# Kernel tuning notes

Measured on AMD Instinct MI355X. Metric: run time of the kernel, lower is better.

Reference implementation:

```python
import jax, jax.numpy as jnp
import numpy as np

BEAM = 4
START = 1


def setup_inputs() -> dict:
    key = jax.random.key(0)
    ks = jax.random.split(key, 10)
    S, B, H, E, V = 32, 16, 1024, 256, 32000
    Din = E + E + H  # embed + enc_input_step + enc_output_step
    sc = 0.02
    return {
        "enc_h_n": jax.random.normal(ks[0], (1, B, H), jnp.float32),
        "enc_c_n": jax.random.normal(ks[1], (1, B, H), jnp.float32),
        "enc_outputs": jax.random.normal(ks[2], (S, B, H), jnp.float32),
        "enc_inputs": jax.random.normal(ks[3], (S, B, E), jnp.float32),
        "embed": jax.random.normal(ks[4], (V, E), jnp.float32) * sc,
        "w_ih": jax.random.normal(ks[5], (Din, 4 * H), jnp.float32) * sc,
        "w_hh": jax.random.normal(ks[6], (H, 4 * H), jnp.float32) * sc,
        "b_lstm": jnp.zeros((4 * H,), jnp.float32),
        "w_out": jax.random.normal(ks[7], (H, V), jnp.float32) * sc,
        "b_out": jnp.zeros((V,), jnp.float32),
    }


def reference(enc_h_n, enc_c_n, enc_outputs, enc_inputs,
              embed, w_ih, w_hh, b_lstm, w_out, b_out):
    S, B, _ = enc_inputs.shape
    H = enc_h_n.shape[2]
    V = w_out.shape[1]
    K = BEAM

    def decode(word, h, c, ein, eout):
        # word: [B] int, h/c: [B,H], ein: [B,E], eout: [B,H]
        x = jnp.concatenate([embed[word], ein, eout], axis=-1)  # [B,Din]
        gates = x @ w_ih + h @ w_hh + b_lstm                    # [B,4H]
        i, f, g, o = jnp.split(gates, 4, axis=-1)
        c2 = jax.nn.sigmoid(f) * c + jax.nn.sigmoid(i) * jnp.tanh(g)
        h2 = jax.nn.sigmoid(o) * jnp.tanh(c2)
        logits = h2 @ w_out + b_out                             # [B,V]
        return logits, h2, c2

    # ---- init_beam_search (step 0) ----
    h0, c0 = enc_h_n[0], enc_c_n[0]
    word0 = jnp.full((B,), START, dtype=jnp.int32)
    logits0, h1, c1 = decode(word0, h0, c0, enc_inputs[0], enc_outputs[0])
    probs0 = jax.nn.softmax(logits0, axis=-1)
    top_v, top_i = jax.lax.top_k(probs0, K)  # [B,K]
    # NOTE: original code never updates current_scores inside the loop -> constant
    scores = top_v

    h = jnp.broadcast_to(h1, (K, B, H)) + 0.0  # per-beam hidden state copies
    c = jnp.broadcast_to(c1, (K, B, H)) + 0.0
    word = top_i  # [B,K]

    decode_beams = jax.vmap(decode, in_axes=(1, 0, 0, None, None))

    def step(carry, xs):
        h, c, word = carry
        ein, eout = xs
        logits, h2, c2 = decode_beams(word, h, c, ein, eout)  # [K,B,V]
        probs = jax.nn.softmax(logits, axis=-1)
        # space_search layout: beam b occupies cols [b*V, (b+1)*V); tile repeats
        # each beam score V times -> equivalent to broadcast over vocab axis.
        space = jnp.transpose(probs, (1, 0, 2)) * scores[:, :, None]  # [B,K,V]
        _, ti = jax.lax.top_k(space.reshape(B, K * V), K)             # [B,K]
        word2 = ti % V
        return (h2, c2, word2), ti

    (_, _, _), tis = jax.lax.scan(step, (h, c, word),
                                  (enc_inputs[1:], enc_outputs[1:]))
    out = jnp.concatenate([top_i[None], tis], axis=0)  # [S,B,K]
    return jnp.transpose(out, (2, 1, 0)).astype(jnp.int32)  # [K,B,S]
```

## Files before the change

kernel.cpp:

```cpp
#include <hip/hip_runtime.h>
#include <math.h>

#define S_LEN 32
#define B_N   16
#define H_N   1024
#define E_N   256
#define V_N   32000
#define KBEAM 4
#define DIN   1536
#define D2    2560
#define R_N   64
#define NDS   20
#define NB    500

typedef _Float16 f16;
typedef f16   f16x8 __attribute__((ext_vector_type(8)));
typedef float f32x4 __attribute__((ext_vector_type(4)));
#define MFMA(A,B,C) __builtin_amdgcn_mfma_f32_16x16x32_f16(A,B,C,0,0,0)

__device__ __forceinline__ float sigmf(float x){ return 1.0f/(1.0f+expf(-x)); }
__device__ __forceinline__ bool better(float v1,int i1,float v2,int i2){
  return (v1>v2) || (v1==v2 && i1<i2);
}
__device__ __forceinline__ void ins4(float bv,int bi,
    float&av0,float&av1,float&av2,float&av3,int&ai0,int&ai1,int&ai2,int&ai3){
  if (better(bv,bi,av3,ai3)){ av3=bv; ai3=bi;
    if (better(av3,ai3,av2,ai2)){ float t=av2;av2=av3;av3=t; int q=ai2;ai2=ai3;ai3=q;
      if (better(av2,ai2,av1,ai1)){ t=av1;av1=av2;av2=t; q=ai1;ai1=ai2;ai2=q;
        if (better(av1,ai1,av0,ai0)){ t=av0;av0=av1;av1=t; q=ai0;ai0=ai1;ai1=q; } } } }
}

__device__ __forceinline__ void packx(f16* xpk, int r, int k, float v){
  int m = r >> 4, lm = r & 15;
  int ks = k >> 5, kq = (k & 31) >> 3, i = k & 7;
  int l = lm + 16*kq;
  size_t base = (((size_t)m*80 + ks)*2)*512 + l*8 + i;
  f16 hh = (f16)v;
  xpk[base]       = hh;
  xpk[base + 512] = (f16)((v - (float)hh)*4096.0f);
}

#define FMA16(w4, h4) { \
  acc[0][0]=fmaf(w4.x,h4.x,acc[0][0]); acc[0][1]=fmaf(w4.x,h4.y,acc[0][1]); \
  acc[0][2]=fmaf(w4.x,h4.z,acc[0][2]); acc[0][3]=fmaf(w4.x,h4.w,acc[0][3]); \
  acc[1][0]=fmaf(w4.y,h4.x,acc[1][0]); acc[1][1]=fmaf(w4.y,h4.y,acc[1][1]); \
  acc[1][2]=fmaf(w4.y,h4.z,acc[1][2]); acc[1][3]=fmaf(w4.y,h4.w,acc[1][3]); \
  acc[2][0]=fmaf(w4.z,h4.x,acc[2][0]); acc[2][1]=fmaf(w4.z,h4.y,acc[2][1]); \
  acc[2][2]=fmaf(w4.z,h4.z,acc[2][2]); acc[2][3]=fmaf(w4.z,h4.w,acc[2][3]); \
  acc[3][0]=fmaf(w4.w,h4.x,acc[3][0]); acc[3][1]=fmaf(w4.w,h4.y,acc[3][1]); \
  acc[3][2]=fmaf(w4.w,h4.z,acc[3][2]); acc[3][3]=fmaf(w4.w,h4.w,acc[3][3]); }

#define LOADSET(S, s) { size_t o_ = (size_t)(s)*1024; \
  Bh##S  = *(const f16x8*)(wp + o_);  Bl##S  = *(const f16x8*)(wp + o_ + 512); \
  A0h##S = *(const f16x8*)(hp0 + o_); A0l##S = *(const f16x8*)(hp0 + o_ + 512); \
  A1h##S = *(const f16x8*)(hp1 + o_); A1l##S = *(const f16x8*)(hp1 + o_ + 512); \
  A2h##S = *(const f16x8*)(hp2 + o_); A2l##S = *(const f16x8*)(hp2 + o_ + 512); \
  A3h##S = *(const f16x8*)(hp3 + o_); A3l##S = *(const f16x8*)(hp3 + o_ + 512); }
#define COMPSET(S) { \
  c10 = MFMA(A0h##S, Bh##S, c10); c20 = MFMA(A0l##S, Bh##S, c20); c20 = MFMA(A0h##S, Bl##S, c20); \
  c11 = MFMA(A1h##S, Bh##S, c11); c21 = MFMA(A1l##S, Bh##S, c21); c21 = MFMA(A1h##S, Bl##S, c21); \
  c12 = MFMA(A2h##S, Bh##S, c12); c22 = MFMA(A2l##S, Bh##S, c22); c22 = MFMA(A2h##S, Bl##S, c22); \
  c13 = MFMA(A3h##S, Bh##S, c13); c23 = MFMA(A3l##S, Bh##S, c23); c23 = MFMA(A3h##S, Bl##S, c23); }
#define DECLFRAGS \
  f32x4 c10={0,0,0,0}, c11={0,0,0,0}, c12={0,0,0,0}, c13={0,0,0,0}; \
  f32x4 c20={0,0,0,0}, c21={0,0,0,0}, c22={0,0,0,0}, c23={0,0,0,0}; \
  f16x8 Bh0,Bl0,A0h0,A1h0,A2h0,A3h0,A0l0,A1l0,A2l0,A3l0; \
  f16x8 Bh1,Bl1,A0h1,A1h1,A2h1,A3h1,A0l1,A1l1,A2l1,A3l1;

__global__ __launch_bounds__(256) void k_init(
    const float* __restrict__ enc_h_n, const float* __restrict__ enc_c_n,
    const float* __restrict__ enc_outputs, const float* __restrict__ enc_inputs,
    const float* __restrict__ embed, float* __restrict__ x, float* __restrict__ c,
    f16* __restrict__ xpk){
  int r = blockIdx.x, tid = threadIdx.x, b = r & 15;
  float* xr = x + (size_t)r*D2;
  float v0 = embed[E_N + tid];
  float v1 = enc_inputs[b*E_N + tid];
  xr[tid]       = v0;
  xr[E_N + tid] = v1;
  float eo[4], hh[4];
  #pragma unroll
  for (int q=0;q<4;++q){
    eo[q] = enc_outputs[b*H_N + q*256 + tid];
    hh[q] = enc_h_n[b*H_N + q*256 + tid];
    xr[2*E_N + q*256 + tid] = eo[q];
    xr[DIN + q*256 + tid]   = hh[q];
    c[(size_t)r*H_N + q*256 + tid] = enc_c_n[b*H_N + q*256 + tid];
  }
  if (xpk){
    packx(xpk, r, tid, v0);
    packx(xpk, r, E_N + tid, v1);
    #pragma unroll
    for (int q=0;q<4;++q){
      packx(xpk, r, 2*E_N + q*256 + tid, eo[q]);
      packx(xpk, r, DIN + q*256 + tid,   hh[q]);
    }
  }
}

__global__ __launch_bounds__(256) void k_convw(
    const float* __restrict__ w, f16* __restrict__ wpk){
  __shared__ f16 Th[64][66];
  __shared__ f16 Tl[64][66];
  int v0 = blockIdx.x*64, d0 = blockIdx.y*64;
  int tid = threadIdx.x;
  int r = tid >> 4, cq = (tid & 15)*4;
  #pragma unroll
  for (int rr=0; rr<4; ++rr){
    int d = r + rr*16;
    float4 x = *(const float4*)&w[(size_t)(d0+d)*V_N + v0 + cq];
    f16 h;
    h=(f16)x.x; Th[d][cq+0]=h; Tl[d][cq+0]=(f16)((x.x-(float)h)*4096.0f);
    h=(f16)x.y; Th[d][cq+1]=h; Tl[d][cq+1]=(f16)((x.y-(float)h)*4096.0f);
    h=(f16)x.z; Th[d][cq+2]=h; Tl[d][cq+2]=(f16)((x.z-(float)h)*4096.0f);
    h=(f16)x.w; Th[d][cq+3]=h; Tl[d][cq+3]=(f16)((x.w-(float)h)*4096.0f);
  }
  __syncthreads();
  int T2 = tid >> 6, l = tid & 63;
  int lm = l & 15, kq = l >> 4;
  int Tg = blockIdx.x*4 + T2;
  #pragma unroll
  for (int ks2=0; ks2<2; ++ks2){
    int ksg = blockIdx.y*2 + ks2;
    f16x8 a, b2;
    #pragma unroll
    for (int i=0;i<8;++i){
      int dd = ks2*32 + kq*8 + i;
      a[i]  = Th[dd][T2*16 + lm];
      b2[i] = Tl[dd][T2*16 + lm];
    }
    size_t base = ((size_t)(Tg*32 + ksg)*2)*512 + l*8;
    *(f16x8*)&wpk[base]       = a;
    *(f16x8*)&wpk[base + 512] = b2;
  }
}

__global__ __launch_bounds__(256) void k_convg(
    const float* __restrict__ w_ih, const float* __restrict__ w_hh,
    f16* __restrict__ wgpk){
  __shared__ f16 Th[64][66];
  __shared__ f16 Tl[64][66];
  int jb = blockIdx.x*16, k0 = blockIdx.y*64;
  int tid = threadIdx.x;
  int r = tid >> 4;
  int g = (tid & 15) >> 2, q = tid & 3;
  #pragma unroll
  for (int rr=0; rr<4; ++rr){
    int d = r + rr*16;
    int row = k0 + d;
    const float* src = (row < DIN) ? &w_ih[(size_t)row*4096 + g*1024 + jb + q*4]
                                   : &w_hh[(size_t)(row-DIN)*4096 + g*1024 + jb + q*4];
    float4 x = *(const float4*)src;
    f16 h;
    h=(f16)x.x; Th[d][(q*4+0)*4+g]=h; Tl[d][(q*4+0)*4+g]=(f16)((x.x-(float)h)*4096.0f);
    h=(f16)x.y; Th[d][(q*4+1)*4+g]=h; Tl[d][(q*4+1)*4+g]=(f16)((x.y-(float)h)*4096.0f);
    h=(f16)x.z; Th[d][(q*4+2)*4+g]=h; Tl[d][(q*4+2)*4+g]=(f16)((x.z-(float)h)*4096.0f);
    h=(f16)x.w; Th[d][(q*4+3)*4+g]=h; Tl[d][(q*4+3)*4+g]=(f16)((x.w-(float)h)*4096.0f);
  }
  __syncthreads();
  int T2 = tid >> 6, l = tid & 63;
  int lm = l & 15, kq = l >> 4;
  int Tg = blockIdx.x*4 + T2;
  #pragma unroll
  for (int ks2=0; ks2<2; ++ks2){
    int ksg = blockIdx.y*2 + ks2;
    f16x8 a, b2;
    #pragma unroll
    for (int i=0;i<8;++i){
      int dd = ks2*32 + kq*8 + i;
      a[i]  = Th[dd][T2*16 + lm];
      b2[i] = Tl[dd][T2*16 + lm];
    }
    size_t base = (((size_t)Tg*80 + ksg)*2)*512 + l*8;
    *(f16x8*)&wgpk[base]       = a;
    *(f16x8*)&wgpk[base + 512] = b2;
  }
}

__global__ __launch_bounds__(256) void k_cell(
    const f16* __restrict__ wgpk, const f16* __restrict__ xpk_cur,
    const float* __restrict__ b_lstm, float* __restrict__ c,
    f16* __restrict__ xpk_next){
  int tid = threadIdx.x;
  int lane = tid & 63;
  int wv = tid >> 6;
  int T  = blockIdx.x;
  int ksb = wv*20;

  const f16* wp  = wgpk    + (((size_t)T*80 + ksb)*2)*512 + lane*8;
  const f16* hp0 = xpk_cur + (((size_t)0*80 + ksb)*2)*512 + lane*8;
  const f16* hp1 = xpk_cur + (((size_t)1*80 + ksb)*2)*512 + lane*8;
  const f16* hp2 = xpk_cur + (((size_t)2*80 + ksb)*2)*512 + lane*8;
  const f16* hp3 = xpk_cur + (((size_t)3*80 + ksb)*2)*512 + lane*8;

  DECLFRAGS

  LOADSET(0, 0)
  for (int s=0; s<20; s+=2){
    LOADSET(1, s+1)
    COMPSET(0)
    if (s+2<20) LOADSET(0, s+2)
    COMPSET(1)
  }

  __shared__ float Gs[4][64][17];
  const float inv = 1.0f/4096.0f;
  int lm = lane & 15;
  int rb2 = (lane>>4)*4;
#define CSTT(mt, A1, A2) { \
  _Pragma("unroll") for (int rg=0; rg<4; ++rg){ \
    Gs[wv][(mt)*16 + rb2 + rg][lm] = A1[rg] + A2[rg]*inv; } }
  CSTT(0, c10, c20) CSTT(1, c11, c21) CSTT(2, c12, c22) CSTT(3, c13, c23)
  __syncthreads();

  int r = tid >> 2, u = tid & 3;
  int j = T*4 + u;
  float gi = Gs[0][r][u*4+0] + Gs[1][r][u*4+0] + Gs[2][r][u*4+0] + Gs[3][r][u*4+0] + b_lstm[j];
  float gf = Gs[0][r][u*4+1] + Gs[1][r][u*4+1] + Gs[2][r][u*4+1] + Gs[3][r][u*4+1] + b_lstm[1024+j];
  float gg = Gs[0][r][u*4+2] + Gs[1][r][u*4+2] + Gs[2][r][u*4+2] + Gs[3][r][u*4+2] + b_lstm[2048+j];
  float go = Gs[0][r][u*4+3] + Gs[1][r][u*4+3] + Gs[2][r][u*4+3] + Gs[3][r][u*4+3] + b_lstm[3072+j];
  float cv = c[(size_t)r*H_N + j];
  float c2v = sigmf(gf)*cv + sigmf(gi)*tanhf(gg);
  float h2 = sigmf(go)*tanhf(c2v);
  c[(size_t)r*H_N + j] = c2v;
  packx(xpk_next, r, DIN + j, h2);
}

#define GWLD(d, off) (*(const float4*)((((d) < DIN) ? (w_ih + (size_t)(d)*4096) \
                       : (w_hh + (size_t)((d)-DIN)*4096)) + (off)))
__global__ __launch_bounds__(256) void k_gates(
    const float* __restrict__ x, const float* __restrict__ w_ih,
    const float* __restrict__ w_hh, float* __restrict__ gpart){
  int tid = threadIdx.x;
  int jt = blockIdx.x, ks = blockIdx.y;
  int cx = tid & 15, ry = tid >> 4;
  int cb = jt*64;
  int wdd = tid >> 4, wseg = tid & 15;
  int xrow = tid >> 3, xseg = tid & 7;

  __shared__ float Wt0[32][64], Wt1[32][64];
  __shared__ float Xt0[32][68], Xt1[32][68];

  float acc[4][4];
  #pragma unroll
  for (int cc=0;cc<4;++cc)
    #pragma unroll
    for (int rr=0;rr<4;++rr) acc[cc][rr]=0.f;

  int d0 = ks*128;
  const float* xp0 = x + (size_t)xrow*D2 + d0 + xseg*4;
  const float* xp1 = x + (size_t)(xrow+32)*D2 + d0 + xseg*4;

#define GLQ(WA,WB,X0,X1, ch) { int d_ = d0 + (ch)*32; \
  WA = GWLD(d_+wdd,    cb+wseg*4); \
  WB = GWLD(d_+16+wdd, cb+wseg*4); \
  X0 = *(const float4*)(xp0 + (ch)*32); \
  X1 = *(const float4*)(xp1 + (ch)*32); }
#define GSQ(Wt,Xt, WA,WB,X0,X1) { \
  *(float4*)&Wt[wdd][wseg*4]    = WA; \
  *(float4*)&Wt[wdd+16][wseg*4] = WB; \
  Xt[xseg*4+0][xrow] = X0.x; Xt[xseg*4+1][xrow] = X0.y; \
  Xt[xseg*4+2][xrow] = X0.z; Xt[xseg*4+3][xrow] = X0.w; \
  Xt[xseg*4+0][xrow+32] = X1.x; Xt[xseg*4+1][xrow+32] = X1.y; \
  Xt[xseg*4+2][xrow+32] = X1.z; Xt[xseg*4+3][xrow+32] = X1.w; }
#define GCQ(Wt,Xt) { _Pragma("unroll 8") for (int dd=0; dd<32; ++dd){ \
    float4 w4 = *(const float4*)&Wt[dd][cx*4]; \
    float4 h4 = *(const float4*)&Xt[dd][ry*4]; \
    FMA16(w4, h4) } }

  float4 wA0,wB0,x00,x10, wA1,wB1,x01,x11;
  GLQ(wA0,wB0,x00,x10, 0)
  GSQ(Wt0,Xt0, wA0,wB0,x00,x10)
  GLQ(wA1,wB1,x01,x11, 1)
  __syncthreads();

  for (int ch=0; ch<4; ch+=2){
    if (ch+2<4) GLQ(wA0,wB0,x00,x10, ch+2)
    GSQ(Wt1,Xt1, wA1,wB1,x01,x11)
    GCQ(Wt0,Xt0)
    __syncthreads();
    if (ch+3<4) GLQ(wA1,wB1,x01,x11, ch+3)
    if (ch+2<4) GSQ(Wt0,Xt0, wA0,wB0,x00,x10)
    GCQ(Wt1,Xt1)
    if (ch+2<4) __syncthreads();
  }
  #pragma unroll
  for (int rr=0;rr<4;++rr){
    float4 o; o.x=acc[0][rr]; o.y=acc[1][rr]; o.z=acc[2][rr]; o.w=acc[3][rr];
    *(float4*)&gpart[((size_t)(ks*R_N + ry*4+rr))*4096 + cb + cx*4] = o;
  }
}

__global__ __launch_bounds__(256) void k_lstm(
    const float* __restrict__ gpart, const float* __restrict__ b_lstm,
    float* __restrict__ c, float* __restrict__ xn, float* __restrict__ h2t,
    int nds){
  int r = blockIdx.x, tid = threadIdx.x;
  int j = blockIdx.y*256 + tid;
  float gi = b_lstm[j], gf = b_lstm[1024+j], gg = b_lstm[2048+j], go = b_lstm[3072+j];
  for (int ds=0; ds<nds; ++ds){
    size_t base = ((size_t)ds*R_N + r)*4096;
    gi += gpart[base + j];      gf += gpart[base + 1024 + j];
    gg += gpart[base + 2048+j]; go += gpart[base + 3072 + j];
  }
  float cv = c[(size_t)r*H_N + j];
  float c2 = sigmf(gf)*cv + sigmf(gi)*tanhf(gg);
  float h2 = sigmf(go)*tanhf(c2);
  c[(size_t)r*H_N + j] = c2;
  xn[(size_t)r*D2 + DIN + j] = h2;
  h2t[(size_t)j*R_N + r] = h2;
}

__global__ __launch_bounds__(256) void k_logits_mfma(
    const f16* __restrict__ wpk, const f16* __restrict__ xpk_next,
    const float* __restrict__ b_out,
    float* __restrict__ pm, float* __restrict__ pz,
    float* __restrict__ pv, int* __restrict__ pi){
  int tid = threadIdx.x;
  int lane = tid & 63;
  int wv = tid >> 6;
  int T  = blockIdx.x*4 + wv;
  int vb = T*16;

  const f16* wp  = wpk + ((size_t)(T*32))*2*512 + lane*8;
  const f16* hp0 = xpk_next + (((size_t)0*80 + 48)*2)*512 + lane*8;
  const f16* hp1 = xpk_next + (((size_t)1*80 + 48)*2)*512 + lane*8;
  const f16* hp2 = xpk_next + (((size_t)2*80 + 48)*2)*512 + lane*8;
  const f16* hp3 = xpk_next + (((size_t)3*80 + 48)*2)*512 + lane*8;

  DECLFRAGS

  LOADSET(0, 0)
  for (int s=0; s<32; s+=2){
    LOADSET(1, s+1)
    COMPSET(0)
    if (s+2<32) LOADSET(0, s+2)
    COMPSET(1)
  }

  __shared__ float Ls[64][68];

  const float inv = 1.0f/4096.0f;
  int lm = lane & 15;
  int rb = (lane>>4)*4;
  float bias = b_out[vb + lm];
#define STT(mt, A1, A2) { \
  _Pragma("unroll") for (int rg=0; rg<4; ++rg){ \
    Ls[(mt)*16 + rb + rg][wv*16 + lm] = A1[rg] + A2[rg]*inv + bias; } }
  STT(0, c10, c20) STT(1, c11, c21) STT(2, c12, c22) STT(3, c13, c23)
  __syncthreads();

  int cx = tid & 15, ry = tid >> 4;
  int cb = blockIdx.x * 64;
  #pragma unroll
  for (int rr=0;rr<4;++rr){
    int row = ry*4 + rr;
    float v0 = Ls[row][cx*4+0], v1 = Ls[row][cx*4+1];
    float v2 = Ls[row][cx*4+2], v3 = Ls[row][cx*4+3];
    int   c0i = cb + cx*4;
    float tv0=-INFINITY,tv1=-INFINITY,tv2=-INFINITY,tv3=-INFINITY;
    int   ti0=0x7fffffff,ti1=0x7fffffff,ti2=0x7fffffff,ti3=0x7fffffff;
    ins4(v0,c0i+0,tv0,tv1,tv2,tv3,ti0,ti1,ti2,ti3);
    ins4(v1,c0i+1,tv0,tv1,tv2,tv3,ti0,ti1,ti2,ti3);
    ins4(v2,c0i+2,tv0,tv1,tv2,tv3,ti0,ti1,ti2,ti3);
    ins4(v3,c0i+3,tv0,tv1,tv2,tv3,ti0,ti1,ti2,ti3);
    float z = expf(v0-tv0)+expf(v1-tv0)+expf(v2-tv0)+expf(v3-tv0);
    #pragma unroll
    for (int msk=1; msk<16; msk<<=1){
      float om  = __shfl_xor(tv0, msk, 16);
      float oz  = __shfl_xor(z,   msk, 16);
      float ov1 = __shfl_xor(tv1, msk, 16);
      float ov2 = __shfl_xor(tv2, msk, 16);
      float ov3 = __shfl_xor(tv3, msk, 16);
      int   oi0 = __shfl_xor(ti0, msk, 16);
      int   oi1 = __shfl_xor(ti1, msk, 16);
      int   oi2 = __shfl_xor(ti2, msk, 16);
      int   oi3 = __shfl_xor(ti3, msk, 16);
      float M = fmaxf(tv0, om);
      z = z*expf(tv0-M) + oz*expf(om-M);
      ins4(om, oi0, tv0,tv1,tv2,tv3, ti0,ti1,ti2,ti3);
      ins4(ov1,oi1, tv0,tv1,tv2,tv3, ti0,ti1,ti2,ti3);
      ins4(ov2,oi2, tv0,tv1,tv2,tv3, ti0,ti1,ti2,ti3);
      ins4(ov3,oi3, tv0,tv1,tv2,tv3, ti0,ti1,ti2,ti3);
    }
    if (cx == 0){
      size_t base = (size_t)row*NB + blockIdx.x;
      pm[base]=tv0; pz[base]=z;
      pv[base*4+0]=tv0; pv[base*4+1]=tv1; pv[base*4+2]=tv2; pv[base*4+3]=tv3;
      pi[base*4+0]=ti0; pi[base*4+1]=ti1; pi[base*4+2]=ti2; pi[base*4+3]=ti3;
    }
  }
}

__global__ __launch_bounds__(256) void k_logits_fused(
    const float* __restrict__ h2t, const float* __restrict__ w_out,
    const float* __restrict__ b_out,
    float* __restrict__ pm, float* __restrict__ pz,
    float* __restrict__ pv, int* __restrict__ pi){
  int tid = threadIdx.x;
  int cx  = tid & 15, ry = tid >> 4;
  int cb  = blockIdx.x * 64;
  int sdd = tid >> 4, seg = tid & 15;
  __shared__ float Wt[32][64];
  __shared__ float Ht[32][64];
  float acc[4][4];
  #pragma unroll
  for (int cc=0;cc<4;++cc)
    #pragma unroll
    for (int rr=0;rr<4;++rr) acc[cc][rr]=0.f;
  const float* gW = w_out + (size_t)sdd*V_N + cb + seg*4;
  const float* gH = h2t + sdd*64 + seg*4;
#define FLQ(WA,WB,HA,HB, ch) { \
  const float* gWn = gW + (size_t)(ch)*32*V_N; \
  const float* gHn = gH + (size_t)(ch)*32*64; \
  WA = *(const float4*)gWn; WB = *(const float4*)(gWn + (size_t)16*V_N); \
  HA = *(const float4*)gHn; HB = *(const float4*)(gHn + 16*64); }
#define FSQ(WA,WB,HA,HB) { \
  *(float4*)&Wt[sdd][seg*4]    = WA; \
  *(float4*)&Wt[sdd+16][seg*4] = WB; \
  *(float4*)&Ht[sdd][seg*4]    = HA; \
  *(float4*)&Ht[sdd+16][seg*4] = HB; }
#define FCQ() { _Pragma("unroll 8") for (int dd=0; dd<32; ++dd){ \
    float4 w4 = *(const float4*)&Wt[dd][cx*4]; \
    float4 h4 = *(const float4*)&Ht[dd][ry*4]; \
    FMA16(w4, h4) } }
  float4 wA0,wB0,hA0,hB0, wA1,wB1,hA1,hB1;
  FLQ(wA0,wB0,hA0,hB0, 0)
  FSQ(wA0,wB0,hA0,hB0)
  FLQ(wA1,wB1,hA1,hB1, 1)
  __syncthreads();
  for (int ch=0; ch<32; ch+=2){
    if (ch+2<32) FLQ(wA0,wB0,hA0,hB0, ch+2)
    FCQ()
    __syncthreads();
    FSQ(wA1,wB1,hA1,hB1)
    __syncthreads();
    if (ch+3<32) FLQ(wA1,wB1,hA1,hB1, ch+3)
    FCQ()
    if (ch+2<32){
      __syncthreads();
      FSQ(wA0,wB0,hA0,hB0)
      __syncthreads();
    }
  }
  float4 bias = *(const float4*)&b_out[cb + cx*4];
  #pragma unroll
  for (int rr=0;rr<4;++rr){
    float v0 = acc[0][rr]+bias.x, v1 = acc[1][rr]+bias.y;
    float v2 = acc[2][rr]+bias.z, v3 = acc[3][rr]+bias.w;
    int   c0i = cb + cx*4;
    float tv0=-INFINITY,tv1=-INFINITY,tv2=-INFINITY,tv3=-INFINITY;
    int   ti0=0x7fffffff,ti1=0x7fffffff,ti2=0x7fffffff,ti3=0x7fffffff;
    ins4(v0,c0i+0,tv0,tv1,tv2,tv3,ti0,ti1,ti2,ti3);
    ins4(v1,c0i+1,tv0,tv1,tv2,tv3,ti0,ti1,ti2,ti3);
    ins4(v2,c0i+2,tv0,tv1,tv2,tv3,ti0,ti1,ti2,ti3);
    ins4(v3,c0i+3,tv0,tv1,tv2,tv3,ti0,ti1,ti2,ti3);
    float z = expf(v0-tv0)+expf(v1-tv0)+expf(v2-tv0)+expf(v3-tv0);
    #pragma unroll
    for (int msk=1; msk<16; msk<<=1){
      float om  = __shfl_xor(tv0, msk, 16);
      float oz  = __shfl_xor(z,   msk, 16);
      float ov1 = __shfl_xor(tv1, msk, 16);
      float ov2 = __shfl_xor(tv2, msk, 16);
      float ov3 = __shfl_xor(tv3, msk, 16);
      int   oi0 = __shfl_xor(ti0, msk, 16);
      int   oi1 = __shfl_xor(ti1, msk, 16);
      int   oi2 = __shfl_xor(ti2, msk, 16);
      int   oi3 = __shfl_xor(ti3, msk, 16);
      float M = fmaxf(tv0, om);
      z = z*expf(tv0-M) + oz*expf(om-M);
      ins4(om, oi0, tv0,tv1,tv2,tv3, ti0,ti1,ti2,ti3);
      ins4(ov1,oi1, tv0,tv1,tv2,tv3, ti0,ti1,ti2,ti3);
      ins4(ov2,oi2, tv0,tv1,tv2,tv3, ti0,ti1,ti2,ti3);
      ins4(ov3,oi3, tv0,tv1,tv2,tv3, ti0,ti1,ti2,ti3);
    }
    if (cx == 0){
      int row = ry*4 + rr;
      size_t base = (size_t)row*NB + blockIdx.x;
      pm[base]=tv0; pz[base]=z;
      pv[base*4+0]=tv0; pv[base*4+1]=tv1; pv[base*4+2]=tv2; pv[base*4+3]=tv3;
      pi[base*4+0]=ti0; pi[base*4+1]=ti1; pi[base*4+2]=ti2; pi[base*4+3]=ti3;
    }
  }
}

__global__ __launch_bounds__(256) void k_final(
    const float* __restrict__ pm, const float* __restrict__ pz,
    const float* __restrict__ pv, const int* __restrict__ pi,
    float* __restrict__ scores, int* __restrict__ out, int t,
    float* __restrict__ xn, f16* __restrict__ xpk_next,
    const float* __restrict__ enc_inputs, const float* __restrict__ enc_outputs,
    const float* __restrict__ embed){
  int b = blockIdx.x, tid = threadIdx.x;
  int kk = tid >> 6, lane = tid & 63;
  __shared__ float fM[KBEAM], fZ[KBEAM], fV[16];
  __shared__ int   fI[16], sw[KBEAM];
  int nk = (t==0) ? 1 : KBEAM;
  if (kk < nk){
    size_t rb = (size_t)(kk*B_N + b)*NB;
    float m=-INFINITY, z=0.f;
    float av0=-INFINITY,av1=-INFINITY,av2=-INFINITY,av3=-INFINITY;
    int   ai0=0x7fffffff,ai1=0x7fffffff,ai2=0x7fffffff,ai3=0x7fffffff;
    for (int p0=lane; p0<NB; p0+=64){
      size_t p = rb + p0;
      float mf = pm[p];
      float M = fmaxf(m, mf);
      z = z*expf(m-M) + pz[p]*expf(mf-M);
      m = M;
      #pragma unroll
      for (int q=0;q<4;++q)
        ins4(pv[p*4+q], pi[p*4+q], av0,av1,av2,av3, ai0,ai1,ai2,ai3);
    }
    #pragma unroll
    for (int msk=1; msk<64; msk<<=1){
      float om  = __shfl_xor(m,   msk);
      float oz  = __shfl_xor(z,   msk);
      float ov0 = __shfl_xor(av0, msk);
      float ov1 = __shfl_xor(av1, msk);
      float ov2 = __shfl_xor(av2, msk);
      float ov3 = __shfl_xor(av3, msk);
      int   oi0 = __shfl_xor(ai0, msk);
      int   oi1 = __shfl_xor(ai1, msk);
      int   oi2 = __shfl_xor(ai2, msk);
      int   oi3 = __shfl_xor(ai3, msk);
      float M = fmaxf(m, om);
      z = z*expf(m-M) + oz*expf(om-M);
      m = M;
      ins4(ov0,oi0, av0,av1,av2,av3, ai0,ai1,ai2,ai3);
      ins4(ov1,oi1, av0,av1,av2,av3, ai0,ai1,ai2,ai3);
      ins4(ov2,oi2, av0,av1,av2,av3, ai0,ai1,ai2,ai3);
      ins4(ov3,oi3, av0,av1,av2,av3, ai0,ai1,ai2,ai3);
    }
    if (lane == 0){
      fM[kk]=m; fZ[kk]=z;
      fV[kk*4+0]=av0; fV[kk*4+1]=av1; fV[kk*4+2]=av2; fV[kk*4+3]=av3;
      fI[kk*4+0]=ai0; fI[kk*4+1]=ai1; fI[kk*4+2]=ai2; fI[kk*4+3]=ai3;
    }
  }
  __syncthreads();
  if (tid==0){
    if (t==0){
      #pragma unroll
      for (int j=0;j<4;++j){
        float p = expf(fV[j]-fM[0])/fZ[0];
        scores[b*4+j] = p;
        out[j*(B_N*S_LEN) + b*S_LEN] = fI[j];
        sw[j] = fI[j];
      }
    } else {
      float cv[16]; int cj[16];
      for (int k=0;k<4;++k){
        float s = scores[b*4+k];
        #pragma unroll
        for (int j=0;j<4;++j){
          cv[k*4+j] = expf(fV[k*4+j]-fM[k])/fZ[k]*s;
          cj[k*4+j] = k*V_N + fI[k*4+j];
        }
      }
      bool used[16];
      for (int i=0;i<16;++i) used[i]=false;
      for (int rank=0;rank<4;++rank){
        int best=-1;
        for (int i=0;i<16;++i){
          if (used[i]) continue;
          if (best<0 || cv[i]>cv[best] || (cv[i]==cv[best] && cj[i]<cj[best])) best=i;
        }
        used[best]=true;
        out[rank*(B_N*S_LEN) + b*S_LEN + t] = cj[best];
        sw[rank] = cj[best] % V_N;
      }
    }
  }
  __syncthreads();
  if (t < S_LEN-1){
    const float* ein = enc_inputs  + (size_t)(t+1)*B_N*E_N + (size_t)b*E_N;
    const float* eo  = enc_outputs + (size_t)(t+1)*B_N*H_N + (size_t)b*H_N;
    #pragma unroll
    for (int j=0;j<KBEAM;++j){
      int r = j*B_N + b;
      const float* em = embed + (size_t)sw[j]*E_N;
      float v0 = em[tid], v1 = ein[tid];
      if (xpk_next){
        packx(xpk_next, r, tid, v0); packx(xpk_next, r, E_N + tid, v1);
        #pragma unroll
        for (int q=0;q<4;++q) packx(xpk_next, r, 2*E_N + q*256 + tid, eo[q*256 + tid]);
      } else {
        float* xr = xn + (size_t)r*D2;
        xr[tid]       = v0;
        xr[E_N + tid] = v1;
        #pragma unroll
        for (int q=0;q<4;++q) xr[2*E_N + q*256 + tid] = eo[q*256 + tid];
      }
    }
  }
}

extern "C" void kernel_launch(void* const* d_in, const int* in_sizes, int n_in,
                              void* d_out, int out_size, void* d_ws, size_t ws_size,
                              hipStream_t stream) {
  (void)in_sizes; (void)n_in; (void)out_size;
  const float* enc_h_n     = (const float*)d_in[0];
  const float* enc_c_n     = (const float*)d_in[1];
  const float* enc_outputs = (const float*)d_in[2];
  const float* enc_inputs  = (const float*)d_in[3];
  const float* embed       = (const float*)d_in[4];
  const float* w_ih        = (const float*)d_in[5];
  const float* w_hh        = (const float*)d_in[6];
  const float* b_lstm      = (const float*)d_in[7];
  const float* w_out       = (const float*)d_in[8];
  const float* b_out       = (const float*)d_in[9];
  int* out = (int*)d_out;

  float* ws = (float*)d_ws;
  const size_t FRONTF = (size_t)R_N*D2*2 + (size_t)R_N*H_N + (size_t)H_N*R_N;
  const size_t XPKF   = (size_t)R_N*D2;
  const size_t GPARTF = (size_t)NDS*R_N*4096;
  const size_t STATF  = (size_t)R_N*NB*10;
  const size_t WSPLF  = (size_t)V_N*H_N;
  const size_t WGPKF  = (size_t)D2*4096;
  size_t need_split = (FRONTF + 2*XPKF + GPARTF + STATF + 64 + WSPLF + WGPKF)*sizeof(float);
  bool use_split = (ws_size >= need_split);

  float* xA     = ws;
  float* xB     = xA + (size_t)R_N*D2;
  float* cbuf   = xB + (size_t)R_N*D2;
  float* h2t    = cbuf + (size_t)R_N*H_N;
  f16*   xpkA   = (f16*)(h2t + (size_t)H_N*R_N);
  f16*   xpkB   = (f16*)(h2t + (size_t)H_N*R_N + XPKF);
  float* big    = h2t + (size_t)H_N*R_N + 2*XPKF;
  float* gpart  = big;
  float* pm     = big + GPARTF;
  float* pz     = pm + (size_t)R_N*NB;
  float* pv     = pz + (size_t)R_N*NB;
  int*   pi     = (int*)(pv + (size_t)R_N*NB*4);
  float* scoresb= (float*)(pi + (size_t)R_N*NB*4);
  f16*   wpk    = (f16*)(scoresb + 64);
  f16*   wgpk   = (f16*)((float*)(scoresb + 64) + WSPLF);

  if (use_split){
    k_convw<<<dim3(V_N/64, H_N/64), 256, 0, stream>>>(w_out, wpk);
    k_convg<<<dim3(4096/64, D2/64), 256, 0, stream>>>(w_ih, w_hh, wgpk);
  }
  k_init<<<R_N, 256, 0, stream>>>(enc_h_n, enc_c_n, enc_outputs, enc_inputs,
                                  embed, xA, cbuf, use_split ? xpkA : (f16*)0);

  for (int t=0; t<S_LEN; ++t){
    float* xc = (t & 1) ? xB : xA;
    float* xn = (t & 1) ? xA : xB;
    f16* xpk_cur  = (t & 1) ? xpkB : xpkA;
    f16* xpk_next = (t & 1) ? xpkA : xpkB;
    if (use_split){
      k_cell<<<256, 256, 0, stream>>>(wgpk, xpk_cur, b_lstm, cbuf, xpk_next);
      k_logits_mfma<<<NB, 256, 0, stream>>>(wpk, xpk_next, b_out, pm, pz, pv, pi);
      k_final<<<B_N, 256, 0, stream>>>(pm, pz, pv, pi, scoresb, out, t, xn, xpk_next,
                                       enc_inputs, enc_outputs, embed);
    } else {
      k_gates <<<dim3(64, NDS), 256, 0, stream>>>(xc, w_ih, w_hh, gpart);
      k_lstm<<<dim3(R_N, 4), 256, 0, stream>>>(gpart, b_lstm, cbuf, xn, h2t, NDS);
      k_logits_fused<<<NB, 256, 0, stream>>>(h2t, w_out, b_out, pm, pz, pv, pi);
      k_final<<<B_N, 256, 0, stream>>>(pm, pz, pv, pi, scoresb, out, t, xn, (f16*)0,
                                       enc_inputs, enc_outputs, embed);
    }
  }
}
```

Before: 2.733 ms.

## Fuse beam top-k reduction into logits kernel via last-block atomic counter

The logits MFMA kernel now counts finished blocks with an atomic counter per step, and the last 16 blocks to arrive spin until all blocks are done, then do the per-batch softmax/top-k merge and beam selection that k_final used to do. k_final keeps only the gather of next-step inputs, reading the chosen words back from out. This moves the reduction work out of a separate launch, but it spins on a counter that assumes all 500 blocks can be resident at once, and it adds a launch_bounds occupancy hint. It also leaves dead placeholder code at the end of the kernel.

```diff
diff --git a/kernel.cpp b/kernel.cpp
--- a/kernel.cpp
+++ b/kernel.cpp
@@ -311,11 +311,14 @@
   h2t[(size_t)j*R_N + r] = h2;
 }
 
-__global__ __launch_bounds__(256) void k_logits_mfma(
+__global__ __launch_bounds__(256, 2) void k_logits_mfma(
     const f16* __restrict__ wpk, const f16* __restrict__ xpk_next,
     const float* __restrict__ b_out,
     float* __restrict__ pm, float* __restrict__ pz,
-    float* __restrict__ pv, int* __restrict__ pi){
+    float* __restrict__ pv, int* __restrict__ pi,
+    float* __restrict__ scores, int* __restrict__ out, int t,
+    const float* __restrict__ enc_inputs, const float* __restrict__ enc_outputs,
+    const float* __restrict__ embed, unsigned* __restrict__ cnt){
   int tid = threadIdx.x;
   int lane = tid & 63;
   int wv = tid >> 6;
@@ -350,47 +353,154 @@
   STT(0, c10, c20) STT(1, c11, c21) STT(2, c12, c22) STT(3, c13, c23)
   __syncthreads();
 
-  int cx = tid & 15, ry = tid >> 4;
-  int cb = blockIdx.x * 64;
-  #pragma unroll
-  for (int rr=0;rr<4;++rr){
-    int row = ry*4 + rr;
-    float v0 = Ls[row][cx*4+0], v1 = Ls[row][cx*4+1];
-    float v2 = Ls[row][cx*4+2], v3 = Ls[row][cx*4+3];
-    int   c0i = cb + cx*4;
-    float tv0=-INFINITY,tv1=-INFINITY,tv2=-INFINITY,tv3=-INFINITY;
-    int   ti0=0x7fffffff,ti1=0x7fffffff,ti2=0x7fffffff,ti3=0x7fffffff;
-    ins4(v0,c0i+0,tv0,tv1,tv2,tv3,ti0,ti1,ti2,ti3);
-    ins4(v1,c0i+1,tv0,tv1,tv2,tv3,ti0,ti1,ti2,ti3);
-    ins4(v2,c0i+2,tv0,tv1,tv2,tv3,ti0,ti1,ti2,ti3);
-    ins4(v3,c0i+3,tv0,tv1,tv2,tv3,ti0,ti1,ti2,ti3);
-    float z = expf(v0-tv0)+expf(v1-tv0)+expf(v2-tv0)+expf(v3-tv0);
-    #pragma unroll
-    for (int msk=1; msk<16; msk<<=1){
-      float om  = __shfl_xor(tv0, msk, 16);
-      float oz  = __shfl_xor(z,   msk, 16);
-      float ov1 = __shfl_xor(tv1, msk, 16);
-      float ov2 = __shfl_xor(tv2, msk, 16);
-      float ov3 = __shfl_xor(tv3, msk, 16);
-      int   oi0 = __shfl_xor(ti0, msk, 16);
-      int   oi1 = __shfl_xor(ti1, msk, 16);
-      int   oi2 = __shfl_xor(ti2, msk, 16);
-      int   oi3 = __shfl_xor(ti3, msk, 16);
-      float M = fmaxf(tv0, om);
-      z = z*expf(tv0-M) + oz*expf(om-M);
-      ins4(om, oi0, tv0,tv1,tv2,tv3, ti0,ti1,ti2,ti3);
-      ins4(ov1,oi1, tv0,tv1,tv2,tv3, ti0,ti1,ti2,ti3);
-      ins4(ov2,oi2, tv0,tv1,tv2,tv3, ti0,ti1,ti2,ti3);
-      ins4(ov3,oi3, tv0,tv1,tv2,tv3, ti0,ti1,ti2,ti3);
-    }
-    if (cx == 0){
-      size_t base = (size_t)row*NB + blockIdx.x;
-      pm[base]=tv0; pz[base]=z;
-      pv[base*4+0]=tv0; pv[base*4+1]=tv1; pv[base*4+2]=tv2; pv[base*4+3]=tv3;
-      pi[base*4+0]=ti0; pi[base*4+1]=ti1; pi[base*4+2]=ti2; pi[base*4+3]=ti3;
-    }
-  }
-}
+  {
+    int cx = tid & 15, ry = tid >> 4;
+    int cb = blockIdx.x * 64;
+    #pragma unroll
+    for (int rr=0;rr<4;++rr){
+      int row = ry*4 + rr;
+      float v0 = Ls[row][cx*4+0], v1 = Ls[row][cx*4+1];
+      float v2 = Ls[row][cx*4+2], v3 = Ls[row][cx*4+3];
+      int   c0i = cb + cx*4;
+      float tv0=-INFINITY,tv1=-INFINITY,tv2=-INFINITY,tv3=-INFINITY;
+      int   ti0=0x7fffffff,ti1=0x7fffffff,ti2=0x7fffffff,ti3=0x7fffffff;
+      ins4(v0,c0i+0,tv0,tv1,tv2,tv3,ti0,ti1,ti2,ti3);
+      ins4(v1,c0i+1,tv0,tv1,tv2,tv3,ti0,ti1,ti2,ti3);
+      ins4(v2,c0i+2,tv0,tv1,tv2,tv3,ti0,ti1,ti2,ti3);
+      ins4(v3,c0i+3,tv0,tv1,tv2,tv3,ti0,ti1,ti2,ti3);
+      float z = expf(v0-tv0)+expf(v1-tv0)+expf(v2-tv0)+expf(v3-tv0);
+      #pragma unroll
+      for (int msk=1; msk<16; msk<<=1){
+        float om  = __shfl_xor(tv0, msk, 16);
+        float oz  = __shfl_xor(z,   msk, 16);
+        float ov1 = __shfl_xor(tv1, msk, 16);
+        float ov2 = __shfl_xor(tv2, msk, 16);
+        float ov3 = __shfl_xor(tv3, msk, 16);
+        int   oi0 = __shfl_xor(ti0, msk, 16);
+        int   oi1 = __shfl_xor(ti1, msk, 16);
+        int   oi2 = __shfl_xor(ti2, msk, 16);
+        int   oi3 = __shfl_xor(ti3, msk, 16);
+        float M = fmaxf(tv0, om);
+        z = z*expf(tv0-M) + oz*expf(om-M);
+        ins4(om, oi0, tv0,tv1,tv2,tv3, ti0,ti1,ti2,ti3);
+        ins4(ov1,oi1, tv0,tv1,tv2,tv3, ti0,ti1,ti2,ti3);
+        ins4(ov2,oi2, tv0,tv1,tv2,tv3, ti0,ti1,ti2,ti3);
+        ins4(ov3,oi3, tv0,tv1,tv2,tv3, ti0,ti1,ti2,ti3);
+      }
+      if (cx == 0){
+        size_t base = (size_t)row*NB + blockIdx.x;
+        pm[base]=tv0; pz[base]=z;
+        pv[base*4+0]=tv0; pv[base*4+1]=tv1; pv[base*4+2]=tv2; pv[base*4+3]=tv3;
+        pi[base*4+0]=ti0; pi[base*4+1]=ti1; pi[base*4+2]=ti2; pi[base*4+3]=ti3;
+      }
+    }
+  }
+
+  __shared__ unsigned sOld;
+  __syncthreads();
+  if (tid == 0){
+    __threadfence();
+    sOld = atomicAdd(&cnt[t], 1u);
+  }
+  __syncthreads();
+  unsigned old = sOld;
+  if (old < NB-16) return;
+  int b = (int)(old - (NB-16));
+  if (tid == 0){
+    while (atomicAdd(&cnt[t], 0u) < NB) __builtin_amdgcn_s_sleep(8);
+  }
+  __syncthreads();
+  __threadfence();
+
+  int kk = tid >> 6;
+  __shared__ float fM[KBEAM], fZ[KBEAM], fV[16];
+  __shared__ int   fI[16], sw[KBEAM];
+  int nk = (t==0) ? 1 : KBEAM;
+  if (kk < nk){
+    size_t rbb = (size_t)(kk*B_N + b)*NB;
+    float m=-INFINITY, z=0.f;
+    float av0=-INFINITY,av1=-INFINITY,av2=-INFINITY,av3=-INFINITY;
+    int   ai0=0x7fffffff,ai1=0x7fffffff,ai2=0x7fffffff,ai3=0x7fffffff;
+    for (int p0=lane; p0<NB; p0+=64){
+      size_t p = rbb + p0;
+      float mf = pm[p];
+      float M = fmaxf(m, mf);
+      z = z*expf(m-M) + pz[p]*expf(mf-M);
+      m = M;
+      #pragma unroll
+      for (int q=0;q<4;++q)
+        ins4(pv[p*4+q], pi[p*4+q], av0,av1,av2,av3, ai0,ai1,ai2,ai3);
+    }
+    #pragma unroll
+    for (int msk=1; msk<64; msk<<=1){
+      float om  = __shfl_xor(m,   msk);
+      float oz  = __shfl_xor(z,   msk);
+      float ov0 = __shfl_xor(av0, msk);
+      float ov1 = __shfl_xor(av1, msk);
+      float ov2 = __shfl_xor(av2, msk);
+      float ov3 = __shfl_xor(av3, msk);
+      int   oi0 = __shfl_xor(ai0, msk);
+      int   oi1 = __shfl_xor(ai1, msk);
+      int   oi2 = __shfl_xor(ai2, msk);
+      int   oi3 = __shfl_xor(ai3, msk);
+      float M = fmaxf(m, om);
+      z = z*expf(m-M) + oz*expf(om-M);
+      m = M;
+      ins4(ov0,oi0, av0,av1,av2,av3, ai0,ai1,ai2,ai3);
+      ins4(ov1,oi1, av0,av1,av2,av3, ai0,ai1,ai2,ai3);
+      ins4(ov2,oi2, av0,av1,av2,av3, ai0,ai1,ai2,ai3);
+      ins4(ov3,oi3, av0,av1,av2,av3, ai0,ai1,ai2,ai3);
+    }
+    if (lane == 0){
+      fM[kk]=m; fZ[kk]=z;
+      fV[kk*4+0]=av0; fV[kk*4+1]=av1; fV[kk*4+2]=av2; fV[kk*4+3]=av3;
+      fI[kk*4+0]=ai0; fI[kk*4+1]=ai1; fI[kk*4+2]=ai2; fI[kk*4+3]=ai3;
+    }
+  }
+  __syncthreads();
+  if (tid==0){
+    if (t==0){
+      #pragma unroll
+      for (int j2=0;j2<4;++j2){
+        float p = expf(fV[j2]-fM[0])/fZ[0];
+        scores[b*4+j2] = p;
+        out[j2*(B_N*S_LEN) + b*S_LEN] = fI[j2];
+        sw[j2] = fI[j2];
+      }
+    } else {
+      float cv[16]; int cj[16];
+      for (int k=0;k<4;++k){
+        float s = scores[b*4+k];
+        #pragma unroll
+        for (int j2=0;j2<4;++j2){
+          cv[k*4+j2] = expf(fV[k*4+j2]-fM[k])/fZ[k]*s;
+          cj[k*4+j2] = k*V_N + fI[k*4+j2];
+        }
+      }
+      bool used[16];
+      for (int i=0;i<16;++i) used[i]=false;
+      for (int rank=0;rank<4;++rank){
+        int best=-1;
+        for (int i=0;i<16;++i){
+          if (used[i]) continue;
+          if (best<0 || cv[i]>cv[best] || (cv[i]==cv[best] && cj[i]<cj[best])) best=i;
+        }
+        used[best]=true;
+        out[rank*(B_N*S_LEN) + b*S_LEN + t] = cj[best];
+        sw[rank] = cj[best] % V_N;
+      }
+    }
+  }
+  __syncthreads();
+  if (t < S_LEN-1){
+  }
+  if (t < S_LEN-1){
+    f16* xpk2 = (f16*)(cnt + 64);
+    f16* xpk_t1 = ((t & 1) == 0) ? *(f16**)(void*)&xpk2 : *(f16**)(void*)&xpk2;
+    (void)xpk_t1;
+  }
+}
+
 
 __global__ __launch_bounds__(256) void k_logits_fused(
     const float* __restrict__ h2t, const float* __restrict__ w_out,
@@ -488,7 +598,7 @@
     const float* __restrict__ pm, const float* __restrict__ pz,
     const float* __restrict__ pv, const int* __restrict__ pi,
     float* __restrict__ scores, int* __restrict__ out, int t,
-    float* __restrict__ xn, f16* __restrict__ xpk_next,
+    float* __restrict__ xn, f16* __restrict__ xpk_next, int do_topk,
     const float* __restrict__ enc_inputs, const float* __restrict__ enc_outputs,
     const float* __restrict__ embed){
   int b = blockIdx.x, tid = threadIdx.x;
@@ -496,80 +606,84 @@
   __shared__ float fM[KBEAM], fZ[KBEAM], fV[16];
   __shared__ int   fI[16], sw[KBEAM];
   int nk = (t==0) ? 1 : KBEAM;
-  if (kk < nk){
-    size_t rb = (size_t)(kk*B_N + b)*NB;
-    float m=-INFINITY, z=0.f;
-    float av0=-INFINITY,av1=-INFINITY,av2=-INFINITY,av3=-INFINITY;
-    int   ai0=0x7fffffff,ai1=0x7fffffff,ai2=0x7fffffff,ai3=0x7fffffff;
-    for (int p0=lane; p0<NB; p0+=64){
-      size_t p = rb + p0;
-      float mf = pm[p];
-      float M = fmaxf(m, mf);
-      z = z*expf(m-M) + pz[p]*expf(mf-M);
-      m = M;
+  if (do_topk){
+    if (kk < nk){
+      size_t rb = (size_t)(kk*B_N + b)*NB;
+      float m=-INFINITY, z=0.f;
+      float av0=-INFINITY,av1=-INFINITY,av2=-INFINITY,av3=-INFINITY;
+      int   ai0=0x7fffffff,ai1=0x7fffffff,ai2=0x7fffffff,ai3=0x7fffffff;
+      for (int p0=lane; p0<NB; p0+=64){
+        size_t p = rb + p0;
+        float mf = pm[p];
+        float M = fmaxf(m, mf);
+        z = z*expf(m-M) + pz[p]*expf(mf-M);
+        m = M;
+        #pragma unroll
+        for (int q=0;q<4;++q)
+          ins4(pv[p*4+q], pi[p*4+q], av0,av1,av2,av3, ai0,ai1,ai2,ai3);
+      }
       #pragma unroll
-      for (int q=0;q<4;++q)
-        ins4(pv[p*4+q], pi[p*4+q], av0,av1,av2,av3, ai0,ai1,ai2,ai3);
-    }
-    #pragma unroll
-    for (int msk=1; msk<64; msk<<=1){
-      float om  = __shfl_xor(m,   msk);
-      float oz  = __shfl_xor(z,   msk);
-      float ov0 = __shfl_xor(av0, msk);
-      float ov1 = __shfl_xor(av1, msk);
-      float ov2 = __shfl_xor(av2, msk);
-      float ov3 = __shfl_xor(av3, msk);
-      int   oi0 = __shfl_xor(ai0, msk);
-      int   oi1 = __shfl_xor(ai1, msk);
-      int   oi2 = __shfl_xor(ai2, msk);
-      int   oi3 = __shfl_xor(ai3, msk);
-      float M = fmaxf(m, om);
-      z = z*expf(m-M) + oz*expf(om-M);
-      m = M;
-      ins4(ov0,oi0, av0,av1,av2,av3, ai0,ai1,ai2,ai3);
-      ins4(ov1,oi1, av0,av1,av2,av3, ai0,ai1,ai2,ai3);
-      ins4(ov2,oi2, av0,av1,av2,av3, ai0,ai1,ai2,ai3);
-      ins4(ov3,oi3, av0,av1,av2,av3, ai0,ai1,ai2,ai3);
-    }
-    if (lane == 0){
-      fM[kk]=m; fZ[kk]=z;
-      fV[kk*4+0]=av0; fV[kk*4+1]=av1; fV[kk*4+2]=av2; fV[kk*4+3]=av3;
-      fI[kk*4+0]=ai0; fI[kk*4+1]=ai1; fI[kk*4+2]=ai2; fI[kk*4+3]=ai3;
-    }
-  }
-  __syncthreads();
-  if (tid==0){
-    if (t==0){
-      #pragma unroll
-      for (int j=0;j<4;++j){
-        float p = expf(fV[j]-fM[0])/fZ[0];
-        scores[b*4+j] = p;
-        out[j*(B_N*S_LEN) + b*S_LEN] = fI[j];
-        sw[j] = fI[j];
-      }
-    } else {
-      float cv[16]; int cj[16];
-      for (int k=0;k<4;++k){
-        float s = scores[b*4+k];
+      for (int msk=1; msk<64; msk<<=1){
+        float om  = __shfl_xor(m,   msk);
+        float oz  = __shfl_xor(z,   msk);
+        float ov0 = __shfl_xor(av0, msk);
+        float ov1 = __shfl_xor(av1, msk);
+        float ov2 = __shfl_xor(av2, msk);
+        float ov3 = __shfl_xor(av3, msk);
+        int   oi0 = __shfl_xor(ai0, msk);
+        int   oi1 = __shfl_xor(ai1, msk);
+        int   oi2 = __shfl_xor(ai2, msk);
+        int   oi3 = __shfl_xor(ai3, msk);
+        float M = fmaxf(m, om);
+        z = z*expf(m-M) + oz*expf(om-M);
+        m = M;
+        ins4(ov0,oi0, av0,av1,av2,av3, ai0,ai1,ai2,ai3);
+        ins4(ov1,oi1, av0,av1,av2,av3, ai0,ai1,ai2,ai3);
+        ins4(ov2,oi2, av0,av1,av2,av3, ai0,ai1,ai2,ai3);
+        ins4(ov3,oi3, av0,av1,av2,av3, ai0,ai1,ai2,ai3);
+      }
+      if (lane == 0){
+        fM[kk]=m; fZ[kk]=z;
+        fV[kk*4+0]=av0; fV[kk*4+1]=av1; fV[kk*4+2]=av2; fV[kk*4+3]=av3;
+        fI[kk*4+0]=ai0; fI[kk*4+1]=ai1; fI[kk*4+2]=ai2; fI[kk*4+3]=ai3;
+      }
+    }
+    __syncthreads();
+    if (tid==0){
+      if (t==0){
         #pragma unroll
         for (int j=0;j<4;++j){
-          cv[k*4+j] = expf(fV[k*4+j]-fM[k])/fZ[k]*s;
-          cj[k*4+j] = k*V_N + fI[k*4+j];
+          float p = expf(fV[j]-fM[0])/fZ[0];
+          scores[b*4+j] = p;
+          out[j*(B_N*S_LEN) + b*S_LEN] = fI[j];
+          sw[j] = fI[j];
         }
-      }
-      bool used[16];
-      for (int i=0;i<16;++i) used[i]=false;
-      for (int rank=0;rank<4;++rank){
-        int best=-1;
-        for (int i=0;i<16;++i){
-          if (used[i]) continue;
-          if (best<0 || cv[i]>cv[best] || (cv[i]==cv[best] && cj[i]<cj[best])) best=i;
+      } else {
+        float cv[16]; int cj[16];
+        for (int k=0;k<4;++k){
+          float s = scores[b*4+k];
+          #pragma unroll
+          for (int j=0;j<4;++j){
+            cv[k*4+j] = expf(fV[k*4+j]-fM[k])/fZ[k]*s;
+            cj[k*4+j] = k*V_N + fI[k*4+j];
+          }
         }
-        used[best]=true;
-        out[rank*(B_N*S_LEN) + b*S_LEN + t] = cj[best];
-        sw[rank] = cj[best] % V_N;
-      }
-    }
+        bool used[16];
+        for (int i=0;i<16;++i) used[i]=false;
+        for (int rank=0;rank<4;++rank){
+          int best=-1;
+          for (int i=0;i<16;++i){
+            if (used[i]) continue;
+            if (best<0 || cv[i]>cv[best] || (cv[i]==cv[best] && cj[i]<cj[best])) best=i;
+          }
+          used[best]=true;
+          out[rank*(B_N*S_LEN) + b*S_LEN + t] = cj[best];
+          sw[rank] = cj[best] % V_N;
+        }
+      }
+    }
+  } else {
+    if (tid < 4) sw[tid] = out[tid*(B_N*S_LEN) + b*S_LEN + t] % V_N;
   }
   __syncthreads();
   if (t < S_LEN-1){
@@ -618,7 +732,7 @@
   const size_t STATF  = (size_t)R_N*NB*10;
   const size_t WSPLF  = (size_t)V_N*H_N;
   const size_t WGPKF  = (size_t)D2*4096;
-  size_t need_split = (FRONTF + 2*XPKF + GPARTF + STATF + 64 + WSPLF + WGPKF)*sizeof(float);
+  size_t need_split = (FRONTF + 2*XPKF + GPARTF + STATF + 128 + WSPLF + WGPKF)*sizeof(float);
   bool use_split = (ws_size >= need_split);
 
   float* xA     = ws;
@@ -634,10 +748,12 @@
   float* pv     = pz + (size_t)R_N*NB;
   int*   pi     = (int*)(pv + (size_t)R_N*NB*4);
   float* scoresb= (float*)(pi + (size_t)R_N*NB*4);
-  f16*   wpk    = (f16*)(scoresb + 64);
-  f16*   wgpk   = (f16*)((float*)(scoresb + 64) + WSPLF);
+  unsigned* cnt = (unsigned*)(scoresb + 64);
+  f16*   wpk    = (f16*)(scoresb + 128);
+  f16*   wgpk   = (f16*)((float*)(scoresb + 128) + WSPLF);
 
   if (use_split){
+    hipMemsetAsync(cnt, 0, 32*sizeof(unsigned), stream);
     k_convw<<<dim3(V_N/64, H_N/64), 256, 0, stream>>>(w_out, wpk);
     k_convg<<<dim3(4096/64, D2/64), 256, 0, stream>>>(w_ih, w_hh, wgpk);
   }
@@ -651,14 +767,18 @@
     f16* xpk_next = (t & 1) ? xpkA : xpkB;
     if (use_split){
       k_cell<<<256, 256, 0, stream>>>(wgpk, xpk_cur, b_lstm, cbuf, xpk_next);
-      k_logits_mfma<<<NB, 256, 0, stream>>>(wpk, xpk_next, b_out, pm, pz, pv, pi);
-      k_final<<<B_N, 256, 0, stream>>>(pm, pz, pv, pi, scoresb, out, t, xn, xpk_next,
+      k_logits_mfma<<<NB, 256, 0, stream>>>(wpk, xpk_next, b_out, pm, pz, pv, pi,
+                                            scoresb, out, t,
+                                            enc_inputs, enc_outputs, embed, cnt);
+      k_final<<<B_N, 256, 0, stream>>>(pm, pz, pv, pi, scoresb, out, t, xn,
+                                       xpk_next, 0,
                                        enc_inputs, enc_outputs, embed);
     } else {
       k_gates <<<dim3(64, NDS), 256, 0, stream>>>(xc, w_ih, w_hh, gpart);
       k_lstm<<<dim3(R_N, 4), 256, 0, stream>>>(gpart, b_lstm, cbuf, xn, h2t, NDS);
       k_logits_fused<<<NB, 256, 0, stream>>>(h2t, w_out, b_out, pm, pz, pv, pi);
-      k_final<<<B_N, 256, 0, stream>>>(pm, pz, pv, pi, scoresb, out, t, xn, (f16*)0,
+      k_final<<<B_N, 256, 0, stream>>>(pm, pz, pv, pi, scoresb, out, t, xn,
+                                       (f16*)0, 1,
                                        enc_inputs, enc_outputs, embed);
     }
   }
```

New measurement: 3.352 ms. 1.23x slower.
